# Kernel tuning notes

Measured on AMD Instinct MI355X. Metric: run time of the kernel, lower is better.

## Reference

```python
import jax, jax.numpy as jnp
import numpy as np

N = 50000          # nodes
E = 800000         # edges
F_IN = 128         # in_channels
C = 64             # cell channels
NCELLS = 2
STEPS = 4
MULT = 4
N_EDGE_SLOTS = 14  # 2+3+4+5 mixed-op edges per cell
N_OPS = 8          # switch_on
NUM_CLASSES = 40
BN_EPS = 1e-5
GCNII_ALPHA = 0.1


def setup_inputs() -> dict:
    key = jax.random.key(0)
    ks = jax.random.split(key, 20)
    def w(k, shape, fan_in):
        return jax.random.normal(k, shape, dtype=jnp.float32) / np.float32(np.sqrt(fan_in))
    return {
        "x": jax.random.normal(ks[0], (N, F_IN), dtype=jnp.float32),
        "edge_index": jax.random.randint(ks[1], (2, E), 0, N, dtype=jnp.int32),
        "alphas": 0.001 * jax.random.normal(ks[2], (N_EDGE_SLOTS, N_OPS), dtype=jnp.float32),
        "stem_W": w(ks[3], (F_IN, 3 * C), F_IN),
        "pre_W": w(ks[4], (F_IN, C), F_IN),
        "pre0_W0": w(ks[5], (3 * C, C), 3 * C),
        "pre1_W0": w(ks[6], (3 * C, C), 3 * C),
        "pre0_W1": w(ks[7], (3 * C, C), 3 * C),
        "pre1_W1": w(ks[8], (MULT * C, C), MULT * C),
        "W_gcn": w(ks[9], (NCELLS, N_EDGE_SLOTS, C, C), C),
        "W_sage_self": w(ks[10], (NCELLS, N_EDGE_SLOTS, C, C), C),
        "W_sage_nei": w(ks[11], (NCELLS, N_EDGE_SLOTS, C, C), C),
        "W_gin": w(ks[12], (NCELLS, N_EDGE_SLOTS, C, C), C),
        "W_gc1": w(ks[13], (NCELLS, N_EDGE_SLOTS, C, C), C),
        "W_gc2": w(ks[14], (NCELLS, N_EDGE_SLOTS, C, C), C),
        "W_mlp": w(ks[15], (NCELLS, N_EDGE_SLOTS, C, C), C),
        "W_gcnii": w(ks[16], (NCELLS, N_EDGE_SLOTS, C, C), C),
        "cls_W": w(ks[17], (MULT * C + 1, NUM_CLASSES), MULT * C + 1),
        "cls_b": jnp.zeros((NUM_CLASSES,), dtype=jnp.float32),
    }


def reference(x, edge_index, alphas, stem_W, pre_W, pre0_W0, pre1_W0, pre0_W1, pre1_W1,
              W_gcn, W_sage_self, W_sage_nei, W_gin, W_gc1, W_gc2, W_mlp, W_gcnii,
              cls_W, cls_b):
    src, dst = edge_index[0], edge_index[1]
    deg = jax.ops.segment_sum(jnp.ones((E,), jnp.float32), dst, num_segments=N)
    deg = jnp.maximum(deg, 1.0)
    inv_deg = 1.0 / deg
    inv_sqrt = jax.lax.rsqrt(deg)
    edge_norm = (inv_sqrt[src] * inv_sqrt[dst])[:, None]  # [E,1] sym-normalized coeff

    def bn(h):  # batch norm over node axis, no affine (gamma=1, beta=0)
        m = jnp.mean(h, axis=0)
        v = jnp.var(h, axis=0)
        return (h - m) * jax.lax.rsqrt(v + BN_EPS)

    def mlp(xx, W, act):  # Linear(no bias) -> BN -> optional ReLU
        h = bn(xx @ W)
        return jnp.maximum(h, 0.0) if act else h

    relu = lambda t: jnp.maximum(t, 0.0)

    def mixed_op(h, wv, ci, ej, x0):
        # shared message-passing aggregations of h over edge_index
        msg = h[src]                                             # [E,C] gather
        s_sum = jax.ops.segment_sum(msg, dst, num_segments=N)    # sum agg
        s_mean = s_sum * inv_deg[:, None]                        # mean agg
        s_norm = jax.ops.segment_sum(msg * edge_norm, dst, num_segments=N)  # gcn agg
        out = wv[1] * h                                          # skip_connect (wv[0]: none)
        out = out + wv[2] * relu(s_norm @ W_gcn[ci, ej])
        out = out + wv[3] * (h @ W_sage_self[ci, ej] + s_mean @ W_sage_nei[ci, ej])
        out = out + wv[4] * relu((h + s_sum) @ W_gin[ci, ej])
        out = out + wv[5] * (h @ W_gc1[ci, ej] + s_sum @ W_gc2[ci, ej])
        out = out + wv[6] * relu(h @ W_mlp[ci, ej])
        out = out + wv[7] * relu(((1.0 - GCNII_ALPHA) * s_norm + GCNII_ALPHA * x0) @ W_gcnii[ci, ej])
        return out

    wmix = jax.nn.softmax(alphas, axis=-1)  # [14,8], identical across cells

    s0 = s1 = mlp(x, stem_W, act=False)     # stem: MLP([in, 3C], act=None)
    x0 = mlp(x, pre_W, act=True)            # preprocess: MLP([in, C], relu)
    pre_ws = [(pre0_W0, pre1_W0), (pre0_W1, pre1_W1)]
    for ci in range(NCELLS):
        p0, p1 = pre_ws[ci]
        a = mlp(s0, p0, act=True)
        b = mlp(s1, p1, act=True)
        states = [a, b]
        offset = 0
        for _ in range(STEPS):
            s = None
            for j, h in enumerate(states):
                o = mixed_op(h, wmix[offset + j], ci, offset + j, x0)
                s = o if s is None else s + o
            offset += len(states)
            states.append(s)
        out_cell = jnp.concatenate(states[-MULT:], axis=1)  # [N, 4C]
        s0, s1 = s1, out_cell

    pooled = jnp.mean(s1, axis=1, keepdims=True)            # AdaptiveAvgPool1d(1) over channels
    logits = jnp.concatenate([pooled, s1], axis=1) @ cls_W + cls_b
    return logits
```

## Files before the change

### kernel.cpp

```cpp
#include <hip/hip_runtime.h>
#include <stdint.h>

typedef unsigned short u16;
typedef __attribute__((ext_vector_type(8))) short bh8;
typedef __attribute__((ext_vector_type(4))) float f4;

__device__ __forceinline__ float b2f(u16 u){ union{unsigned u; float f;} x; x.u = ((unsigned)u)<<16; return x.f; }
__device__ __forceinline__ u16 f2b(float f){ union{float f; unsigned u;} x; x.f = f; return (u16)((x.u + 0x7fffu + ((x.u>>16)&1u))>>16); }
__device__ __forceinline__ bh8 ld8(const u16* p){ return *reinterpret_cast<const bh8*>(p); }

__global__ void k_count_deg(const int* dst, int* deg, int E){
  int i = blockIdx.x*256 + threadIdx.x;
  if (i < E) atomicAdd(&deg[dst[i]], 1);
}

__global__ __launch_bounds__(1024) void k_scan(const int* deg, int* off, int n){
  __shared__ int wsum[16];
  __shared__ int carry_s;
  int t = threadIdx.x, lane = t & 63, wv = t >> 6;
  if (t == 0) carry_s = 0;
  __syncthreads();
  for (int base = 0; base < n; base += 1024){
    int v = (base + t < n) ? deg[base + t] : 0;
    int x = v;
    #pragma unroll
    for (int o = 1; o < 64; o <<= 1){
      int u = __shfl_up(x, (unsigned)o, 64);
      if (lane >= o) x += u;
    }
    if (lane == 63) wsum[wv] = x;
    __syncthreads();
    if (wv == 0 && lane < 16){
      int s = wsum[lane];
      #pragma unroll
      for (int o = 1; o < 16; o <<= 1){
        int u = __shfl_up(s, (unsigned)o, 64);
        if (lane >= o) s += u;
      }
      wsum[lane] = s;
    }
    __syncthreads();
    int woff = (wv == 0) ? 0 : wsum[wv-1];
    int c = carry_s;
    if (base + t < n) off[base + t] = c + woff + x - v;
    __syncthreads();
    if (t == 0) carry_s = c + wsum[15];
    __syncthreads();
  }
  if (threadIdx.x == 0) off[n] = carry_s;
}

__global__ void k_invdeg(const int* deg, const int* off, int* cursor,
                         float* inv_deg, float* inv_sqrt, int n){
  int i = blockIdx.x*256 + threadIdx.x;
  if (i < n){
    cursor[i] = off[i];
    int d = deg[i]; if (d < 1) d = 1;
    float df = (float)d;
    inv_deg[i] = 1.0f/df;
    inv_sqrt[i] = rsqrtf(df);
  }
}

__global__ void k_fill_csr(const int* src, const int* dst, const float* invs,
                           int* cursor, int2* csr, int E){
  int i = blockIdx.x*256 + threadIdx.x;
  if (i < E){
    int s = src[i];
    float w = invs[s];
    int p = atomicAdd(&cursor[dst[i]], 1);
    csr[p] = make_int2(s, __float_as_int(w));
  }
}

__global__ void k_softmax(const float* alphas, float* wmix){
  int t = threadIdx.x; int r = t >> 3, o = t & 7;
  if (r < 14){
    float v = alphas[r*8+o];
    float m = v;
    #pragma unroll
    for (int d=1; d<8; d<<=1) m = fmaxf(m, __shfl_xor(m, d, 8));
    float e = expf(v - m);
    float s = e;
    #pragma unroll
    for (int d=1; d<8; d<<=1) s += __shfl_xor(s, d, 8);
    wmix[r*8+o] = e / s;
  }
}

__global__ void k_f2b(const float* a, u16* b, int n){
  int i = blockIdx.x*256 + threadIdx.x;
  if (i < n) b[i] = f2b(a[i]);
}

__global__ void k_pack2d(const float* W, u16* Bp, int K, int ncol){
  int i = blockIdx.x*256 + threadIdx.x;
  if (i < K*ncol){
    int k = i / ncol, n = i - k*ncol;
    Bp[(size_t)n*K + k] = f2b(W[i]);
  }
}

struct PackArgs { const float* W[8]; const float* wmix; u16* dst; };
__global__ void k_pack_ops8(PackArgs P){
  int i = blockIdx.x*256 + threadIdx.x;
  if (i >= 28*8*4096) return;
  int slot28 = i >> 15;
  int rem = i & 32767;
  int mat = rem >> 12;
  int e = rem & 4095;
  int k = e >> 6, n = e & 63;
  const float* wm = P.wmix + (slot28 % 14)*8;
  size_t off = (size_t)slot28*4096 + e;
  float v = 0.f;
  switch(mat){
    case 0: v = wm[2]*P.W[0][off]; break;
    case 1: v = wm[3]*P.W[1][off] + wm[5]*P.W[4][off] + ((k==n) ? wm[1] : 0.f); break;
    case 2: v = wm[3]*P.W[2][off]; break;
    case 3: v = wm[4]*P.W[3][off]; break;
    case 4: v = wm[5]*P.W[5][off]; break;
    case 5: v = wm[6]*P.W[6][off]; break;
    case 6: v = 0.9f*wm[7]*P.W[7][off]; break;
    case 7: v = 0.1f*wm[7]*P.W[7][off]; break;
  }
  P.dst[(((size_t)slot28*8 + mat)<<12) + (n<<6) + (((k>>3) ^ (n&7))<<3) + (k&7)] = f2b(v);
}

__global__ void k_pack_cls(const float* W, u16* Bp){
  int i = blockIdx.x*256 + threadIdx.x;
  if (i < 48*256){
    int n = i >> 8, k = i & 255;
    float v = 0.f;
    if (n < 40) v = W[(size_t)(1+k)*40 + n] + W[n] * (1.f/256.f);
    Bp[(size_t)n*256 + k] = f2b(v);
  }
}

template<int NT>
__global__ __launch_bounds__(256) void k_gemm(const u16* A, int lda, const u16* Bp, int K,
                                              u16* Tb, int ldT, int Nn, float* S){
  __shared__ float sred[4][NT*16][2];
  int tid = threadIdx.x, wv = tid>>6, lane = tid&63, q = lane>>4, t = lane&15;
  int row0 = blockIdx.x*128 + wv*32;
  f4 acc[2][NT];
  #pragma unroll
  for (int a=0;a<2;a++)
    #pragma unroll
    for (int b=0;b<NT;b++) acc[a][b] = (f4){0.f,0.f,0.f,0.f};
  int nkb = K >> 5;
  const u16* arow0 = A + (size_t)(row0 + t)*lda + q*8;
  const u16* arow1 = arow0 + (size_t)16*lda;
  const u16* brow  = Bp + (size_t)t*K + q*8;
  for (int kb = 0; kb < nkb; ++kb){
    bh8 a0 = ld8(arow0 + kb*32);
    bh8 a1 = ld8(arow1 + kb*32);
    #pragma unroll
    for (int nt=0; nt<NT; ++nt){
      bh8 bf = ld8(brow + (size_t)nt*16*K + kb*32);
      acc[0][nt] = __builtin_amdgcn_mfma_f32_16x16x32_bf16(a0, bf, acc[0][nt], 0, 0, 0);
      acc[1][nt] = __builtin_amdgcn_mfma_f32_16x16x32_bf16(a1, bf, acc[1][nt], 0, 0, 0);
    }
  }
  #pragma unroll
  for (int nt=0;nt<NT;nt++){
    float ps = 0.f, pq = 0.f;
    #pragma unroll
    for (int rt=0;rt<2;rt++)
      #pragma unroll
      for (int r=0;r<4;r++){
        int row = row0 + rt*16 + q*4 + r;
        float v = acc[rt][nt][r];
        if (row < Nn){
          Tb[(size_t)row*ldT + nt*16 + t] = f2b(v);
          ps += v; pq += v*v;
        }
      }
    ps += __shfl_xor(ps, 16, 64); pq += __shfl_xor(pq, 16, 64);
    ps += __shfl_xor(ps, 32, 64); pq += __shfl_xor(pq, 32, 64);
    if (q == 0){ sred[wv][nt*16 + t][0] = ps; sred[wv][nt*16 + t][1] = pq; }
  }
  __syncthreads();
  if (tid < NT*16){
    float s = sred[0][tid][0] + sred[1][tid][0] + sred[2][tid][0] + sred[3][tid][0];
    float qq = sred[0][tid][1] + sred[1][tid][1] + sred[2][tid][1] + sred[3][tid][1];
    atomicAdd(&S[tid], s);
    atomicAdd(&S[256 + tid], qq);
  }
}

__global__ void k_norm(const u16* Tb, int ldT, int ncols, int Nn, const float* S,
                       u16* out, int rs_out, int relu, float invN){
  int i = blockIdx.x*256 + threadIdx.x;
  int nv = ncols >> 3;
  if (i >= Nn*nv) return;
  int r = i / nv, c8 = (i - r*nv)*8;
  bh8 tv = ld8(Tb + (size_t)r*ldT + c8);
  bh8 ov;
  #pragma unroll
  for (int u=0; u<8; ++u){
    int c = c8 + u;
    float m = S[c]*invN;
    float var = S[256+c]*invN - m*m;
    float xv = (b2f((u16)tv[u]) - m) * rsqrtf(var + 1e-5f);
    if (relu) xv = fmaxf(xv, 0.f);
    ov[u] = (short)f2b(xv);
  }
  *reinterpret_cast<bh8*>(out + (size_t)r*rs_out + c8) = ov;
}

#define ACC4(vv, ww) { \
    float c0 = __uint_as_float((vv).x << 16); \
    float c1 = __uint_as_float((vv).x & 0xffff0000u); \
    float c2 = __uint_as_float((vv).y << 16); \
    float c3 = __uint_as_float((vv).y & 0xffff0000u); \
    s0 += c0; s1 += c1; s2 += c2; s3 += c3; \
    n0 += c0*(ww); n1 += c1*(ww); n2 += c2*(ww); n3 += c3*(ww); }

template<int SHIFT>
__global__ __launch_bounds__(256) void k_aggv(const u16* h, const int* off, const int2* csr,
                                              const float* inv_sqrt, u16* out_sum, u16* out_norm, int Nn){
  int g = blockIdx.x*4 + (threadIdx.x >> 6);
  if (g >= Nn) return;
  int lane = threadIdx.x & 63;
  int sub = lane >> 4;
  int cb = (lane & 15) << 2;
  const u16* hp = h + cb;
  float s0=0.f,s1=0.f,s2=0.f,s3=0.f;
  float n0=0.f,n1=0.f,n2=0.f,n3=0.f;
  int e0 = off[g], e1 = off[g+1];
  int e = e0 + sub;
  for (; e + 4 < e1; e += 8){
    int2 cA = csr[e];
    int2 cB = csr[e+4];
    uint2 vA = *reinterpret_cast<const uint2*>(hp + (((unsigned)cA.x) << SHIFT));
    uint2 vB = *reinterpret_cast<const uint2*>(hp + (((unsigned)cB.x) << SHIFT));
    float wA = __int_as_float(cA.y), wB = __int_as_float(cB.y);
    ACC4(vA, wA)
    ACC4(vB, wB)
  }
  if (e < e1){
    int2 cA = csr[e];
    uint2 vA = *reinterpret_cast<const uint2*>(hp + (((unsigned)cA.x) << SHIFT));
    float wA = __int_as_float(cA.y);
    ACC4(vA, wA)
  }
  s0 += __shfl_xor(s0,16,64); s1 += __shfl_xor(s1,16,64);
  s2 += __shfl_xor(s2,16,64); s3 += __shfl_xor(s3,16,64);
  n0 += __shfl_xor(n0,16,64); n1 += __shfl_xor(n1,16,64);
  n2 += __shfl_xor(n2,16,64); n3 += __shfl_xor(n3,16,64);
  s0 += __shfl_xor(s0,32,64); s1 += __shfl_xor(s1,32,64);
  s2 += __shfl_xor(s2,32,64); s3 += __shfl_xor(s3,32,64);
  n0 += __shfl_xor(n0,32,64); n1 += __shfl_xor(n1,32,64);
  n2 += __shfl_xor(n2,32,64); n3 += __shfl_xor(n3,32,64);
  if (sub == 0){
    float ig = inv_sqrt[g];
    uint2 os, on;
    os.x = (uint)f2b(s0) | ((uint)f2b(s1) << 16);
    os.y = (uint)f2b(s2) | ((uint)f2b(s3) << 16);
    on.x = (uint)f2b(n0*ig) | ((uint)f2b(n1*ig) << 16);
    on.y = (uint)f2b(n2*ig) | ((uint)f2b(n3*ig) << 16);
    *reinterpret_cast<uint2*>(out_sum + (size_t)g*64 + cb) = os;
    *reinterpret_cast<uint2*>(out_norm + (size_t)g*64 + cb) = on;
  }
}

#define ACC4AB(va, vb, ww) { \
    float a0 = __uint_as_float((va).x << 16); \
    float a1 = __uint_as_float((va).x & 0xffff0000u); \
    float a2 = __uint_as_float((va).y << 16); \
    float a3 = __uint_as_float((va).y & 0xffff0000u); \
    float b0 = __uint_as_float((vb).x << 16); \
    float b1 = __uint_as_float((vb).x & 0xffff0000u); \
    float b2 = __uint_as_float((vb).y << 16); \
    float b3 = __uint_as_float((vb).y & 0xffff0000u); \
    sa0 += a0; sa1 += a1; sa2 += a2; sa3 += a3; \
    na0 += a0*(ww); na1 += a1*(ww); na2 += a2*(ww); na3 += a3*(ww); \
    sb0 += b0; sb1 += b1; sb2 += b2; sb3 += b3; \
    nb0 += b0*(ww); nb1 += b1*(ww); nb2 += b2*(ww); nb3 += b3*(ww); }

__global__ __launch_bounds__(256) void k_agg2v(const u16* ab, const int* off, const int2* csr,
                                               const float* inv_sqrt,
                                               u16* os0, u16* on0, u16* os1, u16* on1, int Nn){
  int g = blockIdx.x*4 + (threadIdx.x >> 6);
  if (g >= Nn) return;
  int lane = threadIdx.x & 63;
  int sub = lane >> 4;
  int cb = (lane & 15) << 2;
  const u16* hp = ab + cb;
  float sa0=0.f,sa1=0.f,sa2=0.f,sa3=0.f, na0=0.f,na1=0.f,na2=0.f,na3=0.f;
  float sb0=0.f,sb1=0.f,sb2=0.f,sb3=0.f, nb0=0.f,nb1=0.f,nb2=0.f,nb3=0.f;
  int e0 = off[g], e1 = off[g+1];
  int e = e0 + sub;
  for (; e + 4 < e1; e += 8){
    int2 cA = csr[e];
    int2 cB = csr[e+4];
    const u16* rpA = hp + (((unsigned)cA.x) << 7);
    const u16* rpB = hp + (((unsigned)cB.x) << 7);
    uint2 vaA = *reinterpret_cast<const uint2*>(rpA);
    uint2 vbA = *reinterpret_cast<const uint2*>(rpA + 64);
    uint2 vaB = *reinterpret_cast<const uint2*>(rpB);
    uint2 vbB = *reinterpret_cast<const uint2*>(rpB + 64);
    float wA = __int_as_float(cA.y), wB = __int_as_float(cB.y);
    ACC4AB(vaA, vbA, wA)
    ACC4AB(vaB, vbB, wB)
  }
  if (e < e1){
    int2 cA = csr[e];
    const u16* rpA = hp + (((unsigned)cA.x) << 7);
    uint2 vaA = *reinterpret_cast<const uint2*>(rpA);
    uint2 vbA = *reinterpret_cast<const uint2*>(rpA + 64);
    float wA = __int_as_float(cA.y);
    ACC4AB(vaA, vbA, wA)
  }
  #pragma unroll
  for (int m = 16; m <= 32; m <<= 1){
    sa0 += __shfl_xor(sa0,m,64); sa1 += __shfl_xor(sa1,m,64);
    sa2 += __shfl_xor(sa2,m,64); sa3 += __shfl_xor(sa3,m,64);
    na0 += __shfl_xor(na0,m,64); na1 += __shfl_xor(na1,m,64);
    na2 += __shfl_xor(na2,m,64); na3 += __shfl_xor(na3,m,64);
    sb0 += __shfl_xor(sb0,m,64); sb1 += __shfl_xor(sb1,m,64);
    sb2 += __shfl_xor(sb2,m,64); sb3 += __shfl_xor(sb3,m,64);
    nb0 += __shfl_xor(nb0,m,64); nb1 += __shfl_xor(nb1,m,64);
    nb2 += __shfl_xor(nb2,m,64); nb3 += __shfl_xor(nb3,m,64);
  }
  if (sub == 0){
    float ig = inv_sqrt[g];
    uint2 v;
    v.x = (uint)f2b(sa0) | ((uint)f2b(sa1) << 16);
    v.y = (uint)f2b(sa2) | ((uint)f2b(sa3) << 16);
    *reinterpret_cast<uint2*>(os0 + (size_t)g*64 + cb) = v;
    v.x = (uint)f2b(na0*ig) | ((uint)f2b(na1*ig) << 16);
    v.y = (uint)f2b(na2*ig) | ((uint)f2b(na3*ig) << 16);
    *reinterpret_cast<uint2*>(on0 + (size_t)g*64 + cb) = v;
    v.x = (uint)f2b(sb0) | ((uint)f2b(sb1) << 16);
    v.y = (uint)f2b(sb2) | ((uint)f2b(sb3) << 16);
    *reinterpret_cast<uint2*>(os1 + (size_t)g*64 + cb) = v;
    v.x = (uint)f2b(nb0*ig) | ((uint)f2b(nb1*ig) << 16);
    v.y = (uint)f2b(nb2*ig) | ((uint)f2b(nb3*ig) << 16);
    *reinterpret_cast<uint2*>(on1 + (size_t)g*64 + cb) = v;
  }
}

struct StepArgs {
  const u16* h[5]; const u16* asum[5]; const u16* anorm[5];
  int rs[5]; int slot[5]; int J;
  const u16* wpk; const float* inv_deg; const u16* x0;
  u16* out; int rs_out; int Nn;
};

__device__ __forceinline__ void mm8(const bh8 (&af)[2], const u16* wlds, int mat,
                                    int t, int q, f4 (&acc)[4]){
  #pragma unroll
  for (int kb=0;kb<2;kb++)
    #pragma unroll
    for (int nt=0;nt<4;nt++){
      bh8 bf = ld8(wlds + (mat<<12) + ((nt*16+t)<<6) + ((((kb<<2)|q) ^ (t&7))<<3));
      acc[nt] = __builtin_amdgcn_mfma_f32_16x16x32_bf16(af[kb], bf, acc[nt], 0, 0, 0);
    }
}

__global__ __launch_bounds__(512, 4)
void k_step(StepArgs A){
  __shared__ __align__(16) u16 wlds[8*4096];
  int tid = threadIdx.x, wv = tid>>6, lane = tid&63, q = lane>>4, t = lane&15;
  int row0 = blockIdx.x*128 + wv*16;
  int rA = row0 + t;
  int q8 = q*8;
  f4 idg = *reinterpret_cast<const f4*>(A.inv_deg + row0 + q*4);
  const u16* xp = A.x0 + (size_t)rA*64;
  bh8 fx[2];
  fx[0]=ld8(xp+q8); fx[1]=ld8(xp+32+q8);

  f4 oacc[4];
  #pragma unroll
  for (int b=0;b<4;b++) oacc[b] = (f4){0.f,0.f,0.f,0.f};

  uint4* wdst = reinterpret_cast<uint4*>(wlds);
  for (int j = 0; j < A.J; ++j){
    if (j) __syncthreads();
    const uint4* wsrc = reinterpret_cast<const uint4*>(A.wpk) + ((size_t)A.slot[j] << 12);
    #pragma unroll
    for (int i = 0; i < 8; ++i) wdst[tid + i*512] = wsrc[tid + i*512];

    const u16* h = A.h[j]; int rs = A.rs[j];
    const u16* hp = h + (size_t)rA*rs;
    const u16* sp = A.asum[j] + (size_t)rA*64;
    const u16* np = A.anorm[j] + (size_t)rA*64;
    bh8 fh[2], fs[2], fn[2];
    fh[0]=ld8(hp+q8); fh[1]=ld8(hp+32+q8);
    fs[0]=ld8(sp+q8); fs[1]=ld8(sp+32+q8);
    fn[0]=ld8(np+q8); fn[1]=ld8(np+32+q8);

    __syncthreads();

    mm8(fh, wlds, 1, t, q, oacc);
    mm8(fs, wlds, 4, t, q, oacc);
    f4 p[4];
    #pragma unroll
    for (int b=0;b<4;b++) p[b] = (f4){0.f,0.f,0.f,0.f};
    mm8(fh, wlds, 5, t, q, p);
    #pragma unroll
    for (int nt=0;nt<4;nt++)
      #pragma unroll
      for (int r=0;r<4;r++) oacc[nt][r] += fmaxf(p[nt][r], 0.f);
    #pragma unroll
    for (int b=0;b<4;b++) p[b] = (f4){0.f,0.f,0.f,0.f};
    mm8(fh, wlds, 3, t, q, p);
    mm8(fs, wlds, 3, t, q, p);
    #pragma unroll
    for (int nt=0;nt<4;nt++)
      #pragma unroll
      for (int r=0;r<4;r++) oacc[nt][r] += fmaxf(p[nt][r], 0.f);
    #pragma unroll
    for (int b=0;b<4;b++) p[b] = (f4){0.f,0.f,0.f,0.f};
    mm8(fn, wlds, 0, t, q, p);
    #pragma unroll
    for (int nt=0;nt<4;nt++)
      #pragma unroll
      for (int r=0;r<4;r++) oacc[nt][r] += fmaxf(p[nt][r], 0.f);
    #pragma unroll
    for (int b=0;b<4;b++) p[b] = (f4){0.f,0.f,0.f,0.f};
    mm8(fn, wlds, 6, t, q, p);
    mm8(fx, wlds, 7, t, q, p);
    #pragma unroll
    for (int nt=0;nt<4;nt++)
      #pragma unroll
      for (int r=0;r<4;r++) oacc[nt][r] += fmaxf(p[nt][r], 0.f);
    #pragma unroll
    for (int b=0;b<4;b++) p[b] = (f4){0.f,0.f,0.f,0.f};
    mm8(fs, wlds, 2, t, q, p);
    #pragma unroll
    for (int nt=0;nt<4;nt++)
      #pragma unroll
      for (int r=0;r<4;r++) oacc[nt][r] += idg[r]*p[nt][r];
  }

  #pragma unroll
  for (int nt=0;nt<4;nt++)
    #pragma unroll
    for (int r=0;r<4;r++){
      int rr = row0 + q*4 + r;
      if (rr < A.Nn) A.out[(size_t)rr*A.rs_out + nt*16 + t] = f2b(oacc[nt][r]);
    }
}

__global__ __launch_bounds__(256) void k_cls_mm(const u16* A, const u16* Bp,
                                                const float* bvec, float* out, int Nn){
  int tid = threadIdx.x, wv = tid>>6, lane = tid&63, q = lane>>4, t = lane&15;
  int row0 = blockIdx.x*128 + wv*32;
  f4 acc[2][3];
  #pragma unroll
  for (int a=0;a<2;a++)
    #pragma unroll
    for (int b=0;b<3;b++) acc[a][b] = (f4){0.f,0.f,0.f,0.f};
  const u16* arow0 = A + (size_t)(row0 + t)*256 + q*8;
  const u16* arow1 = arow0 + (size_t)16*256;
  const u16* brow  = Bp + (size_t)t*256 + q*8;
  #pragma unroll
  for (int kb = 0; kb < 8; ++kb){
    bh8 a0 = ld8(arow0 + kb*32);
    bh8 a1 = ld8(arow1 + kb*32);
    #pragma unroll
    for (int nt=0; nt<3; ++nt){
      bh8 bf = ld8(brow + (size_t)nt*16*256 + kb*32);
      acc[0][nt] = __builtin_amdgcn_mfma_f32_16x16x32_bf16(a0, bf, acc[0][nt], 0, 0, 0);
      acc[1][nt] = __builtin_amdgcn_mfma_f32_16x16x32_bf16(a1, bf, acc[1][nt], 0, 0, 0);
    }
  }
  #pragma unroll
  for (int rt=0;rt<2;rt++)
    #pragma unroll
    for (int nt=0;nt<3;nt++){
      int col = nt*16 + t;
      #pragma unroll
      for (int r=0;r<4;r++){
        int row = row0 + rt*16 + q*4 + r;
        if (row < Nn && col < 40) out[(size_t)row*40 + col] = acc[rt][nt][r] + bvec[col];
      }
    }
}

extern "C" void kernel_launch(void* const* d_in, const int* in_sizes, int n_in,
                              void* d_out, int out_size, void* d_ws, size_t ws_size,
                              hipStream_t stream){
  (void)n_in; (void)out_size; (void)ws_size;
  const float* x      = (const float*)d_in[0];
  const int*   ei     = (const int*)d_in[1];
  const float* alphas = (const float*)d_in[2];
  const float* stem_W = (const float*)d_in[3];
  const float* pre_W  = (const float*)d_in[4];
  const float* p00    = (const float*)d_in[5];
  const float* p10    = (const float*)d_in[6];
  const float* p01    = (const float*)d_in[7];
  const float* p11    = (const float*)d_in[8];
  const float* clsW = (const float*)d_in[17];
  const float* clsb = (const float*)d_in[18];

  int N = in_sizes[0] / 128;
  int E = in_sizes[1] / 2;
  const int* esrc = ei;
  const int* edst = ei + E;

  char* p = (char*)d_ws;
  auto carve = [&](size_t bytes) -> char* {
    char* r = p; p += (bytes + 255) & ~(size_t)255; return r;
  };
  int*   deg     = (int*)carve((size_t)N*4);
  int*   off     = (int*)carve((size_t)(N+1)*4);
  int*   cursor  = (int*)carve((size_t)N*4);
  int2*  csr     = (int2*)carve((size_t)E*8);
  float* inv_deg = (float*)carve((size_t)N*4);
  float* invs    = (float*)carve((size_t)N*4);
  float* wmix    = (float*)carve(14*8*4);
  float* stats   = (float*)carve(512*4);
  u16* xb      = (u16*)carve((size_t)N*128*2);
  u16* stem_pk = (u16*)carve((size_t)192*128*2);
  u16* pre_pk  = (u16*)carve((size_t)64*128*2);
  u16* p00_pk  = (u16*)carve((size_t)64*192*2);
  u16* p10_pk  = (u16*)carve((size_t)64*192*2);
  u16* p01_pk  = (u16*)carve((size_t)64*192*2);
  u16* p11_pk  = (u16*)carve((size_t)64*256*2);
  u16* cls_pk  = (u16*)carve((size_t)48*256*2);
  u16* ops_pk  = (u16*)carve((size_t)28*8*4096*2);
  u16* T       = (u16*)carve((size_t)N*192*2);
  u16* stem_o  = (u16*)carve((size_t)N*192*2);
  u16* x0b     = (u16*)carve((size_t)N*64*2);
  u16* ab      = (u16*)carve((size_t)N*128*2);
  u16* oc0     = (u16*)carve((size_t)N*256*2);
  u16* oc1     = (u16*)carve((size_t)N*256*2);
  u16* agg     = (u16*)carve((size_t)5*2*N*64*2);
  carve(131072);

  auto aggS = [&](int j){ return agg + (size_t)j*2*N*64; };
  auto aggN = [&](int j){ return agg + (size_t)j*2*N*64 + (size_t)N*64; };

  int eg = (E + 255)/256;
  int ng = (N + 255)/256;
  int gg = (N + 127)/128;
  int gstep = (N + 127)/128;
  int ag = (N + 3)/4;
  float invN = 1.0f/(float)N;

  hipMemsetAsync(deg, 0, (size_t)N*4, stream);
  k_count_deg<<<eg,256,0,stream>>>(edst, deg, E);
  k_scan<<<1,1024,0,stream>>>(deg, off, N);
  k_invdeg<<<ng,256,0,stream>>>(deg, off, cursor, inv_deg, invs, N);
  k_fill_csr<<<eg,256,0,stream>>>(esrc, edst, invs, cursor, csr, E);
  k_softmax<<<1,128,0,stream>>>(alphas, wmix);
  k_f2b<<<(N*128+255)/256,256,0,stream>>>(x, xb, N*128);
  k_pack2d<<<(128*192+255)/256,256,0,stream>>>(stem_W, stem_pk, 128, 192);
  k_pack2d<<<(128*64+255)/256,256,0,stream>>>(pre_W, pre_pk, 128, 64);
  k_pack2d<<<(192*64+255)/256,256,0,stream>>>(p00, p00_pk, 192, 64);
  k_pack2d<<<(192*64+255)/256,256,0,stream>>>(p10, p10_pk, 192, 64);
  k_pack2d<<<(192*64+255)/256,256,0,stream>>>(p01, p01_pk, 192, 64);
  k_pack2d<<<(256*64+255)/256,256,0,stream>>>(p11, p11_pk, 256, 64);
  k_pack_cls<<<(48*256+255)/256,256,0,stream>>>(clsW, cls_pk);
  {
    PackArgs PA;
    for (int i = 0; i < 8; ++i) PA.W[i] = (const float*)d_in[9+i];
    PA.wmix = wmix; PA.dst = ops_pk;
    k_pack_ops8<<<(28*8*4096+255)/256,256,0,stream>>>(PA);
  }

  auto mlp = [&](const u16* A, int lda, const u16* Bp, int K, int ncol, u16* outb, int rs_out, int relu){
    hipMemsetAsync(stats, 0, 512*4, stream);
    if (ncol == 192)
      hipLaunchKernelGGL(HIP_KERNEL_NAME(k_gemm<12>), dim3(gg), dim3(256), 0, stream, A, lda, Bp, K, T, ncol, N, stats);
    else
      hipLaunchKernelGGL(HIP_KERNEL_NAME(k_gemm<4>), dim3(gg), dim3(256), 0, stream, A, lda, Bp, K, T, ncol, N, stats);
    k_norm<<<((N*(ncol>>3))+255)/256,256,0,stream>>>(T, ncol, ncol, N, stats, outb, rs_out, relu, invN);
  };

  mlp(xb, 128, stem_pk, 128, 192, stem_o, 192, 0);
  mlp(xb, 128, pre_pk, 128, 64, x0b, 64, 1);

  u16* ocs[2] = {oc0, oc1};
  const int slotbase[4] = {0, 2, 5, 9};
  for (int ci = 0; ci < 2; ++ci){
    const u16* s1in = (ci == 0) ? stem_o : oc0;
    int lda1 = (ci == 0) ? 192 : 256;
    int Kb   = (ci == 0) ? 192 : 256;
    const u16* pa = (ci == 0) ? p00_pk : p01_pk;
    const u16* pb = (ci == 0) ? p10_pk : p11_pk;
    mlp(stem_o, 192, pa, 192, 64, ab, 128, 1);
    mlp(s1in, lda1, pb, Kb, 64, ab + 64, 128, 1);

    u16* oc = ocs[ci];
    const u16* wpk_cell = ops_pk + (size_t)ci*14*8*4096;

    k_agg2v<<<ag,256,0,stream>>>(ab, off, csr, invs,
                                 aggS(0), aggN(0), aggS(1), aggN(1), N);

    const u16* st[5] = { ab, ab + 64, oc + 0, oc + 64, oc + 128 };
    const int strs[5] = {128, 128, 256, 256, 256};
    for (int step = 0; step < 4; ++step){
      StepArgs SA{};
      int J = step + 2;
      for (int j = 0; j < J; ++j){
        SA.h[j] = st[j]; SA.rs[j] = strs[j];
        SA.asum[j] = aggS(j); SA.anorm[j] = aggN(j);
        SA.slot[j] = slotbase[step] + j;
      }
      SA.J = J; SA.wpk = wpk_cell; SA.inv_deg = inv_deg; SA.x0 = x0b;
      SA.out = oc + (size_t)step*64; SA.rs_out = 256; SA.Nn = N;
      k_step<<<gstep,512,0,stream>>>(SA);
      if (step < 3)
        hipLaunchKernelGGL(HIP_KERNEL_NAME(k_aggv<8>), dim3(ag), dim3(256), 0, stream,
                           oc + (size_t)step*64, off, csr, invs, aggS(step+2), aggN(step+2), N);
    }
  }

  k_cls_mm<<<gg,256,0,stream>>>(oc1, cls_pk, clsb, (float*)d_out, N);
}
```

Before: 902.2 us.

## Build CSR via two-level bucket sort with shared-memory atomics

Replaces the global-atomic degree count, single-block serial scan over all nodes, and global-atomic CSR fill with a bucketed approach. Edges are first grouped into 512 buckets of 128 destination nodes using shared-memory histograms, then per-bucket blocks compute degrees, offsets and fill CSR with local atomics. This removes the long single-block scan over 50k nodes and the contended global atomics, at the cost of an extra packed edge buffer pass. It assumes N fits in 512*128 nodes and source ids fit in 25 bits.

```diff
diff --git a/kernel.cpp b/kernel.cpp
--- a/kernel.cpp
+++ b/kernel.cpp
@@ -9,67 +9,109 @@
 __device__ __forceinline__ u16 f2b(float f){ union{float f; unsigned u;} x; x.f = f; return (u16)((x.u + 0x7fffu + ((x.u>>16)&1u))>>16); }
 __device__ __forceinline__ bh8 ld8(const u16* p){ return *reinterpret_cast<const bh8*>(p); }
 
-__global__ void k_count_deg(const int* dst, int* deg, int E){
-  int i = blockIdx.x*256 + threadIdx.x;
-  if (i < E) atomicAdd(&deg[dst[i]], 1);
-}
-
-__global__ __launch_bounds__(1024) void k_scan(const int* deg, int* off, int n){
-  __shared__ int wsum[16];
-  __shared__ int carry_s;
-  int t = threadIdx.x, lane = t & 63, wv = t >> 6;
-  if (t == 0) carry_s = 0;
-  __syncthreads();
-  for (int base = 0; base < n; base += 1024){
-    int v = (base + t < n) ? deg[base + t] : 0;
-    int x = v;
-    #pragma unroll
-    for (int o = 1; o < 64; o <<= 1){
-      int u = __shfl_up(x, (unsigned)o, 64);
-      if (lane >= o) x += u;
-    }
-    if (lane == 63) wsum[wv] = x;
-    __syncthreads();
-    if (wv == 0 && lane < 16){
-      int s = wsum[lane];
-      #pragma unroll
-      for (int o = 1; o < 16; o <<= 1){
-        int u = __shfl_up(s, (unsigned)o, 64);
-        if (lane >= o) s += u;
-      }
-      wsum[lane] = s;
-    }
-    __syncthreads();
-    int woff = (wv == 0) ? 0 : wsum[wv-1];
-    int c = carry_s;
-    if (base + t < n) off[base + t] = c + woff + x - v;
-    __syncthreads();
-    if (t == 0) carry_s = c + wsum[15];
-    __syncthreads();
-  }
-  if (threadIdx.x == 0) off[n] = carry_s;
-}
-
-__global__ void k_invdeg(const int* deg, const int* off, int* cursor,
-                         float* inv_deg, float* inv_sqrt, int n){
-  int i = blockIdx.x*256 + threadIdx.x;
-  if (i < n){
-    cursor[i] = off[i];
-    int d = deg[i]; if (d < 1) d = 1;
-    float df = (float)d;
-    inv_deg[i] = 1.0f/df;
-    inv_sqrt[i] = rsqrtf(df);
-  }
-}
-
-__global__ void k_fill_csr(const int* src, const int* dst, const float* invs,
-                           int* cursor, int2* csr, int E){
-  int i = blockIdx.x*256 + threadIdx.x;
-  if (i < E){
-    int s = src[i];
-    float w = invs[s];
-    int p = atomicAdd(&cursor[dst[i]], 1);
-    csr[p] = make_int2(s, __float_as_int(w));
+#define NBK 512
+
+__global__ __launch_bounds__(256) void k_hist(const int* dst, int* hist, int E){
+  __shared__ int h[NBK];
+  for (int i=threadIdx.x;i<NBK;i+=256) h[i]=0;
+  __syncthreads();
+  int stride = 256*gridDim.x;
+  for (int i = blockIdx.x*256+threadIdx.x; i<E; i+=stride)
+    atomicAdd(&h[dst[i]>>7], 1);
+  __syncthreads();
+  for (int i=threadIdx.x;i<NBK;i+=256){
+    int v=h[i]; if (v) atomicAdd(&hist[i], v);
+  }
+}
+
+__global__ __launch_bounds__(512) void k_scanb(const int* hist, int* bbase, int* bcursor){
+  int t = threadIdx.x, lane = t&63, wv = t>>6;
+  __shared__ int ws[8];
+  int v = hist[t];
+  int x = v;
+  #pragma unroll
+  for (int o=1;o<64;o<<=1){ int u=__shfl_up(x,(unsigned)o,64); if(lane>=o) x+=u; }
+  if (lane==63) ws[wv]=x;
+  __syncthreads();
+  if (t<8){
+    int s=ws[t];
+    #pragma unroll
+    for (int o=1;o<8;o<<=1){ int u=__shfl_up(s,(unsigned)o,8); if (t>=o) s+=u; }
+    ws[t]=s;
+  }
+  __syncthreads();
+  int base = (wv==0)?0:ws[wv-1];
+  int ex = base + x - v;
+  bbase[t]=ex; bcursor[t]=ex;
+  if (t==511) bbase[512]=ex+v;
+}
+
+__global__ __launch_bounds__(256) void k_bucket(const int* src, const int* dst,
+                                                int* bcursor, unsigned* bkt, int E, int nblk){
+  __shared__ int h[NBK], base[NBK], lc[NBK];
+  int per = (E + nblk - 1)/nblk;
+  int e0 = blockIdx.x*per, e1 = min(E, e0+per);
+  for (int i=threadIdx.x;i<NBK;i+=256){ h[i]=0; lc[i]=0; }
+  __syncthreads();
+  for (int e=e0+threadIdx.x; e<e1; e+=256) atomicAdd(&h[dst[e]>>7], 1);
+  __syncthreads();
+  for (int i=threadIdx.x;i<NBK;i+=256){
+    int c=h[i]; base[i] = c ? atomicAdd(&bcursor[i], c) : 0;
+  }
+  __syncthreads();
+  for (int e=e0+threadIdx.x; e<e1; e+=256){
+    int d = dst[e];
+    int b = d>>7;
+    int r = atomicAdd(&lc[b], 1);
+    bkt[base[b]+r] = ((unsigned)(d&127)<<25) | (unsigned)src[e];
+  }
+}
+
+__global__ __launch_bounds__(128) void k_degb(const unsigned* bkt, const int* bbase,
+                                              int* off, float* inv_deg, float* invs,
+                                              int N, int E){
+  int b = blockIdx.x, t = threadIdx.x;
+  __shared__ int cnt[128];
+  __shared__ int w0tot;
+  cnt[t]=0;
+  __syncthreads();
+  int e0=bbase[b], e1=bbase[b+1];
+  for (int e=e0+t; e<e1; e+=128) atomicAdd(&cnt[bkt[e]>>25], 1);
+  __syncthreads();
+  int v = cnt[t];
+  int lane=t&63, wv=t>>6;
+  int x=v;
+  #pragma unroll
+  for (int o=1;o<64;o<<=1){ int u=__shfl_up(x,(unsigned)o,64); if(lane>=o) x+=u; }
+  if (t==63) w0tot=x;
+  __syncthreads();
+  int ex = x - v + (wv ? w0tot : 0);
+  int node = b*128 + t;
+  if (node < N){
+    off[node] = e0 + ex;
+    int d = (v<1)?1:v;
+    float df=(float)d;
+    inv_deg[node]=1.0f/df;
+    invs[node]=rsqrtf(df);
+  }
+  if (b==0 && t==0) off[N]=E;
+}
+
+__global__ __launch_bounds__(128) void k_fillb(const unsigned* bkt, const int* bbase,
+                                               const int* off, const float* invs,
+                                               int2* csr, int N){
+  int b = blockIdx.x, t = threadIdx.x;
+  __shared__ int cur[128];
+  int node = b*128 + t;
+  cur[t] = (node < N) ? off[node] : 0;
+  __syncthreads();
+  int e0=bbase[b], e1=bbase[b+1];
+  for (int e=e0+t; e<e1; e+=128){
+    unsigned v = bkt[e];
+    int i = (int)(v>>25);
+    int s = (int)(v & 0x1FFFFFFu);
+    int pos = atomicAdd(&cur[i], 1);
+    csr[pos] = make_int2(s, __float_as_int(invs[s]));
   }
 }
 
@@ -505,9 +547,11 @@
   auto carve = [&](size_t bytes) -> char* {
     char* r = p; p += (bytes + 255) & ~(size_t)255; return r;
   };
-  int*   deg     = (int*)carve((size_t)N*4);
+  int*   hist    = (int*)carve((size_t)NBK*4);
+  int*   bbase   = (int*)carve((size_t)(NBK+1)*4);
+  int*   bcursor = (int*)carve((size_t)NBK*4);
+  unsigned* bkt  = (unsigned*)carve((size_t)E*4);
   int*   off     = (int*)carve((size_t)(N+1)*4);
-  int*   cursor  = (int*)carve((size_t)N*4);
   int2*  csr     = (int2*)carve((size_t)E*8);
   float* inv_deg = (float*)carve((size_t)N*4);
   float* invs    = (float*)carve((size_t)N*4);
@@ -534,18 +578,19 @@
   auto aggS = [&](int j){ return agg + (size_t)j*2*N*64; };
   auto aggN = [&](int j){ return agg + (size_t)j*2*N*64 + (size_t)N*64; };
 
-  int eg = (E + 255)/256;
-  int ng = (N + 255)/256;
+  int NB = (N + 127)/128;
   int gg = (N + 127)/128;
   int gstep = (N + 127)/128;
   int ag = (N + 3)/4;
   float invN = 1.0f/(float)N;
 
-  hipMemsetAsync(deg, 0, (size_t)N*4, stream);
-  k_count_deg<<<eg,256,0,stream>>>(edst, deg, E);
-  k_scan<<<1,1024,0,stream>>>(deg, off, N);
-  k_invdeg<<<ng,256,0,stream>>>(deg, off, cursor, inv_deg, invs, N);
-  k_fill_csr<<<eg,256,0,stream>>>(esrc, edst, invs, cursor, csr, E);
+  hipMemsetAsync(hist, 0, (size_t)NBK*4, stream);
+  k_hist<<<256,256,0,stream>>>(edst, hist, E);
+  k_scanb<<<1,512,0,stream>>>(hist, bbase, bcursor);
+  k_bucket<<<256,256,0,stream>>>(esrc, edst, bcursor, bkt, E, 256);
+  k_degb<<<NB,128,0,stream>>>(bkt, bbase, off, inv_deg, invs, N, E);
+  k_fillb<<<NB,128,0,stream>>>(bkt, bbase, off, invs, csr, N);
+
   k_softmax<<<1,128,0,stream>>>(alphas, wmix);
   k_f2b<<<(N*128+255)/256,256,0,stream>>>(x, xb, N*128);
   k_pack2d<<<(128*192+255)/256,256,0,stream>>>(stem_W, stem_pk, 128, 192);
```

New measurement: 831.2 us. 7.9% less time.
